# Optimization experiments

Hardware: AMD Instinct MI355X
Metric: run time of the kernel (lower is better)

The kernel has to match this reference:

```python
import jax, jax.numpy as jnp
import numpy as np

B = 8
IMG_H = 128
IMG_W = 128
C = 128
HEADS = 4
WS = 8
SHIFT = 4
HIDDEN = 512
EPS = 1e-5


def _rel_pos_index(ws):
    coords = np.stack(np.meshgrid(np.arange(ws), np.arange(ws), indexing='ij'))  # (2, ws, ws)
    cf = coords.reshape(2, -1)  # (2, N)
    rel = (cf[:, :, None] - cf[:, None, :]).transpose(1, 2, 0).copy()  # (N, N, 2)
    rel[:, :, 0] += ws - 1
    rel[:, :, 1] += ws - 1
    rel[:, :, 0] *= 2 * ws - 1
    return rel.sum(-1)  # (N, N) int


def _win_part_np(x, ws):
    b, h, w, c = x.shape
    x = x.reshape(b, h // ws, ws, w // ws, ws, c).transpose(0, 1, 3, 2, 4, 5)
    return x.reshape(-1, ws, ws, c)


def _attn_mask(H, W, ws, ss):
    img = np.zeros((1, H, W, 1), dtype=np.float32)
    slices = (slice(0, -ws), slice(-ws, -ss), slice(-ss, None))
    cnt = 0
    for hs in slices:
        for wsl in slices:
            img[:, hs, wsl, :] = cnt
            cnt += 1
    mw = _win_part_np(img, ws).reshape(-1, ws * ws)  # (nW, N)
    am = mw[:, None, :] - mw[:, :, None]  # (nW, N, N)
    return np.where(am != 0, np.float32(-100.0), np.float32(0.0))


def _layernorm(x, g, b):
    m = x.mean(-1, keepdims=True)
    v = ((x - m) ** 2).mean(-1, keepdims=True)
    return (x - m) / jnp.sqrt(v + EPS) * g + b


def setup_inputs() -> dict:
    key = jax.random.key(0)
    ks = jax.random.split(key, 8)
    s = 0.02
    return {
        'x': jax.random.normal(ks[0], (B, IMG_H * IMG_W, C), jnp.float32),
        'rpb_table': jax.random.normal(ks[1], ((2 * WS - 1) ** 2, HEADS), jnp.float32) * s,
        'norm1_g': jnp.ones((C,), jnp.float32),
        'norm1_b': jnp.zeros((C,), jnp.float32),
        'qkv_w': jax.random.normal(ks[2], (3 * C, C), jnp.float32) * s,
        'qkv_b': jnp.zeros((3 * C,), jnp.float32),
        'proj_w': jax.random.normal(ks[3], (C, C), jnp.float32) * s,
        'proj_b': jnp.zeros((C,), jnp.float32),
        'norm2_g': jnp.ones((C,), jnp.float32),
        'norm2_b': jnp.zeros((C,), jnp.float32),
        'fc1_w': jax.random.normal(ks[4], (HIDDEN, C), jnp.float32) * s,
        'fc1_b': jnp.zeros((HIDDEN,), jnp.float32),
        'fc2_w': jax.random.normal(ks[5], (C, HIDDEN), jnp.float32) * s,
        'fc2_b': jnp.zeros((C,), jnp.float32),
        'H': IMG_H,
        'W': IMG_W,
    }


def reference(x, rpb_table, norm1_g, norm1_b, qkv_w, qkv_b, proj_w, proj_b,
              norm2_g, norm2_b, fc1_w, fc1_b, fc2_w, fc2_b, H, W):
    Bx, L, Cx = x.shape
    nh, d, ws, ss = HEADS, C // HEADS, WS, SHIFT
    N = ws * ws
    shortcut = x
    h = _layernorm(x, norm1_g, norm1_b).reshape(Bx, H, W, Cx)
    # cyclic shift
    h = jnp.roll(h, (-ss, -ss), axis=(1, 2))
    # window partition -> (nW*B, N, C)
    h = h.reshape(Bx, H // ws, ws, W // ws, ws, Cx).transpose(0, 1, 3, 2, 4, 5).reshape(-1, N, Cx)
    # attention
    qkv = h @ qkv_w.T + qkv_b  # (nW*B, N, 3C)
    qkv = qkv.reshape(-1, N, 3, nh, d).transpose(2, 0, 3, 1, 4)  # (3, nW*B, nh, N, d)
    q, k, v = qkv[0] * (d ** -0.5), qkv[1], qkv[2]
    attn = jnp.einsum('whnd,whmd->whnm', q, k)  # (nW*B, nh, N, N)
    idx = _rel_pos_index(ws)
    bias = rpb_table[idx.reshape(-1)].reshape(N, N, nh).transpose(2, 0, 1)  # (nh, N, N)
    attn = attn + bias[None]
    mask = jnp.asarray(_attn_mask(H, W, ws, ss), x.dtype)  # (nW, N, N)
    nW = mask.shape[0]
    attn = attn.reshape(Bx, nW, nh, N, N) + mask[None, :, None]
    attn = jax.nn.softmax(attn.reshape(-1, nh, N, N), axis=-1)
    out = jnp.einsum('whnm,whmd->whnd', attn, v).transpose(0, 2, 1, 3).reshape(-1, N, Cx)
    out = out @ proj_w.T + proj_b
    # window reverse + reverse shift
    out = out.reshape(Bx, H // ws, W // ws, ws, ws, Cx).transpose(0, 1, 3, 2, 4, 5).reshape(Bx, H, W, Cx)
    out = jnp.roll(out, (ss, ss), axis=(1, 2)).reshape(Bx, H * W, Cx)
    x = shortcut + out
    # MLP with residual
    h2 = _layernorm(x, norm2_g, norm2_b)
    h2 = jax.nn.gelu(h2 @ fc1_w.T + fc1_b, approximate=False)
    h2 = h2 @ fc2_w.T + fc2_b
    return x + h2
```

## Files before the change

### kernel.cpp

```cpp
#include <hip/hip_runtime.h>
#include <math.h>

typedef unsigned short u16;
typedef unsigned int   u32;

#define SS_    4
#define NH     4
#define Dh     32
#define Cdim   128
#define Ntok   64
#define WTOT   2048
#define Mrows  131072
#define HIDDEN 512
#define PSTR   72
#define OSTR   136
#define HPAD   136

typedef __bf16 bf16x8 __attribute__((ext_vector_type(8)));
typedef u16    u16x8  __attribute__((ext_vector_type(8)));
typedef float  f32x4  __attribute__((ext_vector_type(4)));

__device__ __forceinline__ float bf2f(u16 u){
    union {u32 i; float f;} v; v.i = ((u32)u) << 16; return v.f;
}
__device__ __forceinline__ u16 f2bf(float f){
    union {float f; u32 i;} v; v.f = f;
    u32 x = v.i;
    return (u16)((x + 0x7fffu + ((x >> 16) & 1u)) >> 16);
}

__device__ __forceinline__ float fast_gelu(float v){
    float z = v * (1.5957691216057308f + 0.07135481627561976f * v * v);
    return v / (1.0f + __expf(-z));
}

__device__ __forceinline__ int map_row_to_token(int r){
    int w = r >> 6, n = r & 63;
    int b = w >> 8, win = w & 255;
    int wy = win >> 4, wx = win & 15;
    int iy = n >> 3, ix = n & 7;
    int ro = (wy*8 + iy + SS_) & 127;
    int co = (wx*8 + ix + SS_) & 127;
    return (b << 14) + (ro << 7) + co;
}

__device__ __forceinline__ int map_token_to_row(int t){
    int b = t >> 14, ro = (t >> 7) & 127, co = t & 127;
    int y  = (ro + 128 - SS_) & 127;
    int xq = (co + 128 - SS_) & 127;
    return (((b << 8) | ((y >> 3) << 4) | (xq >> 3)) << 6) + (y & 7)*8 + (xq & 7);
}

__global__ void __launch_bounds__(256) cvt_kernel(const float* __restrict__ src,
        u16* __restrict__ dst, int n)
{
    int i = blockIdx.x * 256 + threadIdx.x;
    if (i < n) dst[i] = f2bf(src[i]);
}

__global__ void __launch_bounds__(256) bm_kernel(const float* __restrict__ rpb,
        float* __restrict__ bmt)
{
    int e = blockIdx.x * 256 + threadIdx.x;
    int cls = e >> 14, h = (e >> 12) & 3, row = (e >> 6) & 63, col = e & 63;
    int iy = row >> 3, ix = row & 7, jy = col >> 3, jx = col & 7;
    int bidx = (iy - jy + 7)*15 + (ix - jx + 7);
    float bias = rpb[bidx*NH + h];
    int ybit = cls >> 1, xbit = cls & 1;
    int ri = (ybit ? (iy < 4 ? 1 : 2) : 0)*3 + (xbit ? (ix < 4 ? 1 : 2) : 0);
    int rj = (ybit ? (jy < 4 ? 1 : 2) : 0)*3 + (xbit ? (jx < 4 ? 1 : 2) : 0);
    bmt[e] = bias + ((ri != rj) ? -100.0f : 0.0f);
}

__global__ void __launch_bounds__(512, 4) ln1qkv_kernel(
        const float* __restrict__ x,
        const float* __restrict__ g, const float* __restrict__ bsh,
        const u16* __restrict__ Bw,
        const float* __restrict__ bias,
        u16* __restrict__ qb, u16* __restrict__ kb, u16* __restrict__ vb)
{
    __shared__ __align__(16) u16 Asm[128*HPAD];
    int t = threadIdx.x;
    size_t tilebase = (size_t)blockIdx.x * 128;

    #pragma unroll
    for (int it = 0; it < 4; it++){
        int idx = it*512 + t;
        int rr  = idx >> 4, c8 = idx & 15;
        int trow = (int)tilebase + rr;
        int src  = map_row_to_token(trow);
        f32x4 xa = *(const f32x4*)&x[(size_t)src*Cdim + c8*8];
        f32x4 xb = *(const f32x4*)&x[(size_t)src*Cdim + c8*8 + 4];
        float s = 0.0f, s2 = 0.0f;
        #pragma unroll
        for (int k = 0; k < 4; k++){
            s += xa[k] + xb[k];
            s2 += xa[k]*xa[k] + xb[k]*xb[k];
        }
        #pragma unroll
        for (int off = 1; off <= 8; off <<= 1){
            s  += __shfl_xor(s,  off, 64);
            s2 += __shfl_xor(s2, off, 64);
        }
        float mean = s * (1.0f/128.0f);
        float var  = s2 * (1.0f/128.0f) - mean*mean;
        float inv  = rsqrtf(var + 1e-5f);
        f32x4 ga = *(const f32x4*)&g[c8*8],  gb = *(const f32x4*)&g[c8*8 + 4];
        f32x4 ba = *(const f32x4*)&bsh[c8*8], bb = *(const f32x4*)&bsh[c8*8 + 4];
        u16x8 ov;
        #pragma unroll
        for (int k = 0; k < 4; k++){
            ov[k]   = f2bf((xa[k] - mean) * inv * ga[k] + ba[k]);
            ov[k+4] = f2bf((xb[k] - mean) * inv * gb[k] + bb[k]);
        }
        *(u16x8*)&Asm[rr*HPAD + c8*8] = ov;
    }
    __syncthreads();

    int wave = t >> 6, lane = t & 63;
    int wr = wave & 1, wc = wave >> 1;
    int m = lane & 15, quad = lane >> 4;

    #pragma unroll
    for (int pass = 0; pass < 2; pass++){
        int colbase = wc*96 + pass*48;
        f32x4 acc[4][3] = {};
        #pragma unroll
        for (int s = 0; s < 4; s++){
            bf16x8 aq[4], bk[3];
            #pragma unroll
            for (int i = 0; i < 4; i++)
                aq[i] = *(const bf16x8*)&Asm[(wr*64 + i*16 + m)*HPAD + s*32 + quad*8];
            #pragma unroll
            for (int j = 0; j < 3; j++)
                bk[j] = *(const bf16x8*)&Bw[(size_t)(colbase + j*16 + m)*Cdim
                                            + s*32 + quad*8];
            #pragma unroll
            for (int i = 0; i < 4; i++)
                #pragma unroll
                for (int j = 0; j < 3; j++)
                    acc[i][j] = __builtin_amdgcn_mfma_f32_16x16x32_bf16(
                                    aq[i], bk[j], acc[i][j], 0, 0, 0);
        }

        #pragma unroll
        for (int j = 0; j < 3; j++){
            int c = colbase + j*16 + m;
            float bia = bias[c];
            int which = c >> 7;
            int h = (c >> 5) & 3;
            int d = c & 31;
            #pragma unroll
            for (int i = 0; i < 4; i++){
                #pragma unroll
                for (int rg = 0; rg < 4; rg++){
                    int r = (int)tilebase + wr*64 + i*16 + quad*4 + rg;
                    float v = acc[i][j][rg] + bia;
                    int w = r >> 6, n = r & 63;
                    if (which == 0){
                        qb[((size_t)(w*NH + h)*Ntok + n)*Dh + d] =
                            f2bf(v * 0.17677669529663687f);
                    } else if (which == 1){
                        kb[((size_t)(w*NH + h)*Ntok + n)*Dh + d] = f2bf(v);
                    } else {
                        vb[((size_t)(w*NH + h)*Dh + d)*Ntok + n] = f2bf(v);
                    }
                }
            }
        }
    }
}

__global__ void __launch_bounds__(512, 4) mlp_kernel(
        const float* __restrict__ x,
        const u16* __restrict__ projout,
        const float* __restrict__ g, const float* __restrict__ bsh,
        const u16* __restrict__ W1,
        const float* __restrict__ b1,
        const u16* __restrict__ W2,
        const float* __restrict__ b2,
        float* __restrict__ outp)
{
    __shared__ __align__(16) u16 Asm[128*HPAD];
    __shared__ __align__(16) u16 Hsm[128*HPAD];
    int t = threadIdx.x;
    int wave = t >> 6, lane = t & 63;
    int wr = wave & 1, wc = wave >> 1;
    int m = lane & 15, quad = lane >> 4;
    size_t rowbase = (size_t)blockIdx.x * 128;

    #pragma unroll
    for (int it = 0; it < 4; it++){
        int idx  = it*512 + t;
        int r    = idx >> 4, c8 = idx & 15;
        int trow = (int)rowbase + r;
        int rr   = map_token_to_row(trow);
        f32x4 xa = *(const f32x4*)&x[(size_t)trow*Cdim + c8*8];
        f32x4 xb = *(const f32x4*)&x[(size_t)trow*Cdim + c8*8 + 4];
        u16x8 pv = *(const u16x8*)&projout[(size_t)rr*Cdim + c8*8];
        float val[8];
        float s = 0.0f, s2 = 0.0f;
        #pragma unroll
        for (int k = 0; k < 8; k++){
            float xv = (k < 4) ? xa[k] : xb[k-4];
            val[k] = xv + bf2f(pv[k]);
            s += val[k]; s2 += val[k]*val[k];
        }
        #pragma unroll
        for (int off = 1; off <= 8; off <<= 1){
            s  += __shfl_xor(s,  off, 64);
            s2 += __shfl_xor(s2, off, 64);
        }
        float mean = s * (1.0f/128.0f);
        float var  = s2 * (1.0f/128.0f) - mean*mean;
        float inv  = rsqrtf(var + 1e-5f);
        f32x4 ga = *(const f32x4*)&g[c8*8],  gb = *(const f32x4*)&g[c8*8 + 4];
        f32x4 ba = *(const f32x4*)&bsh[c8*8], bb = *(const f32x4*)&bsh[c8*8 + 4];
        u16x8 ov;
        #pragma unroll
        for (int k = 0; k < 8; k++){
            float gv = (k < 4) ? ga[k] : gb[k-4];
            float bv = (k < 4) ? ba[k] : bb[k-4];
            ov[k] = f2bf((val[k] - mean) * inv * gv + bv);
        }
        *(u16x8*)&Asm[r*HPAD + c8*8] = ov;
    }
    __syncthreads();

    f32x4 O[4][2] = {};

    for (int kk = 0; kk < 4; kk++){
        f32x4 Hacc[4][2] = {};
        #pragma unroll
        for (int s = 0; s < 4; s++){
            bf16x8 aq[4], bk[2];
            #pragma unroll
            for (int i = 0; i < 4; i++)
                aq[i] = *(const bf16x8*)&Asm[(wr*64 + i*16 + m)*HPAD + s*32 + quad*8];
            #pragma unroll
            for (int j = 0; j < 2; j++)
                bk[j] = *(const bf16x8*)&W1[(size_t)(kk*128 + wc*32 + j*16 + m)*Cdim
                                            + s*32 + quad*8];
            #pragma unroll
            for (int i = 0; i < 4; i++)
                #pragma unroll
                for (int j = 0; j < 2; j++)
                    Hacc[i][j] = __builtin_amdgcn_mfma_f32_16x16x32_bf16(
                                     aq[i], bk[j], Hacc[i][j], 0, 0, 0);
        }
        #pragma unroll
        for (int i = 0; i < 4; i++){
            #pragma unroll
            for (int j = 0; j < 2; j++){
                int hc = wc*32 + j*16 + m;
                float bia = b1[kk*128 + hc];
                #pragma unroll
                for (int rg = 0; rg < 4; rg++){
                    int r = wr*64 + i*16 + quad*4 + rg;
                    Hsm[r*HPAD + hc] = f2bf(fast_gelu(Hacc[i][j][rg] + bia));
                }
            }
        }
        __syncthreads();

        #pragma unroll
        for (int s = 0; s < 4; s++){
            bf16x8 pa[4], bk[2];
            #pragma unroll
            for (int i = 0; i < 4; i++)
                pa[i] = *(const bf16x8*)&Hsm[(wr*64 + i*16 + m)*HPAD + s*32 + quad*8];
            #pragma unroll
            for (int j = 0; j < 2; j++)
                bk[j] = *(const bf16x8*)&W2[(size_t)(wc*32 + j*16 + m)*HIDDEN
                                            + kk*128 + s*32 + quad*8];
            #pragma unroll
            for (int i = 0; i < 4; i++)
                #pragma unroll
                for (int j = 0; j < 2; j++)
                    O[i][j] = __builtin_amdgcn_mfma_f32_16x16x32_bf16(
                                  pa[i], bk[j], O[i][j], 0, 0, 0);
        }
        __syncthreads();
    }

    #pragma unroll
    for (int i = 0; i < 4; i++){
        #pragma unroll
        for (int rg = 0; rg < 4; rg++){
            int r  = (int)rowbase + wr*64 + i*16 + quad*4 + rg;
            int rr = map_token_to_row(r);
            #pragma unroll
            for (int j = 0; j < 2; j++){
                int c = wc*32 + j*16 + m;
                float v = x[(size_t)r*Cdim + c] + bf2f(projout[(size_t)rr*Cdim + c])
                          + O[i][j][rg] + b2[c];
                outp[(size_t)r*Cdim + c] = v;
            }
        }
    }
}

__global__ void __launch_bounds__(256) attnproj_kernel(
        const u16* __restrict__ qb, const u16* __restrict__ kb,
        const u16* __restrict__ vt, const float* __restrict__ bmt,
        const u16* __restrict__ pw, const float* __restrict__ pb,
        u16* __restrict__ projout)
{
    __shared__ __align__(16) u16 SH[NH*64*PSTR];
    int w = blockIdx.x;
    int win = w & 255;
    int wy = win >> 4, wx = win & 15;
    int cls = ((wy == 15) ? 2 : 0) | ((wx == 15) ? 1 : 0);
    int t = threadIdx.x;
    int h = t >> 6, lane = t & 63;
    int m = lane & 15, quad = lane >> 4;
    u16* Ph  = SH + h*64*PSTR;
    u16* Osm = SH;

    const u16* qg = qb + (size_t)(w*NH + h)*2048;
    const u16* kg = kb + (size_t)(w*NH + h)*2048;
    const u16* vg = vt + (size_t)(w*NH + h)*2048;
    const float* bm = bmt + (size_t)(cls*NH + h)*4096;

    bf16x8 aq[4], bk[4];
    #pragma unroll
    for (int i = 0; i < 4; i++)
        aq[i] = *(const bf16x8*)&qg[(i*16 + m)*32 + quad*8];
    #pragma unroll
    for (int j = 0; j < 4; j++)
        bk[j] = *(const bf16x8*)&kg[(j*16 + m)*32 + quad*8];
    f32x4 S[4][4] = {};
    #pragma unroll
    for (int i = 0; i < 4; i++)
        #pragma unroll
        for (int j = 0; j < 4; j++)
            S[i][j] = __builtin_amdgcn_mfma_f32_16x16x32_bf16(
                          aq[i], bk[j], S[i][j], 0, 0, 0);

    #pragma unroll
    for (int i = 0; i < 4; i++){
        #pragma unroll
        for (int rg = 0; rg < 4; rg++){
            int row = i*16 + quad*4 + rg;
            float s0 = S[i][0][rg] + bm[row*64 +  0 + m];
            float s1 = S[i][1][rg] + bm[row*64 + 16 + m];
            float s2 = S[i][2][rg] + bm[row*64 + 32 + m];
            float s3 = S[i][3][rg] + bm[row*64 + 48 + m];
            float mx = fmaxf(fmaxf(s0, s1), fmaxf(s2, s3));
            mx = fmaxf(mx, __shfl_xor(mx, 1, 64));
            mx = fmaxf(mx, __shfl_xor(mx, 2, 64));
            mx = fmaxf(mx, __shfl_xor(mx, 4, 64));
            mx = fmaxf(mx, __shfl_xor(mx, 8, 64));
            s0 = __expf(s0 - mx); s1 = __expf(s1 - mx);
            s2 = __expf(s2 - mx); s3 = __expf(s3 - mx);
            float sm = s0 + s1 + s2 + s3;
            sm += __shfl_xor(sm, 1, 64);
            sm += __shfl_xor(sm, 2, 64);
            sm += __shfl_xor(sm, 4, 64);
            sm += __shfl_xor(sm, 8, 64);
            float rinv = 1.0f / sm;
            u16* pr = &Ph[row*PSTR];
            pr[ 0 + m] = f2bf(s0 * rinv);
            pr[16 + m] = f2bf(s1 * rinv);
            pr[32 + m] = f2bf(s2 * rinv);
            pr[48 + m] = f2bf(s3 * rinv);
        }
    }

    f32x4 O[4][2] = {};
    #pragma unroll
    for (int s2 = 0; s2 < 2; s2++){
        bf16x8 pa[4], bv[2];
        #pragma unroll
        for (int i = 0; i < 4; i++)
            pa[i] = *(const bf16x8*)&Ph[(i*16 + m)*PSTR + s2*32 + quad*8];
        #pragma unroll
        for (int dt = 0; dt < 2; dt++)
            bv[dt] = *(const bf16x8*)&vg[(dt*16 + m)*64 + s2*32 + quad*8];
        #pragma unroll
        for (int i = 0; i < 4; i++)
            #pragma unroll
            for (int dt = 0; dt < 2; dt++)
                O[i][dt] = __builtin_amdgcn_mfma_f32_16x16x32_bf16(
                               pa[i], bv[dt], O[i][dt], 0, 0, 0);
    }

    __syncthreads();

    #pragma unroll
    for (int i = 0; i < 4; i++)
        #pragma unroll
        for (int dt = 0; dt < 2; dt++)
            #pragma unroll
            for (int rg = 0; rg < 4; rg++)
                Osm[(i*16 + quad*4 + rg)*OSTR + h*Dh + dt*16 + m] =
                    f2bf(O[i][dt][rg]);
    __syncthreads();

    f32x4 pacc[4][2] = {};
    #pragma unroll
    for (int s = 0; s < 4; s++){
        bf16x8 pa[4], pbk[2];
        #pragma unroll
        for (int i = 0; i < 4; i++)
            pa[i] = *(const bf16x8*)&Osm[(i*16 + m)*OSTR + s*32 + quad*8];
        #pragma unroll
        for (int j = 0; j < 2; j++)
            pbk[j] = *(const bf16x8*)&pw[(size_t)(h*Dh + j*16 + m)*Cdim
                                         + s*32 + quad*8];
        #pragma unroll
        for (int i = 0; i < 4; i++)
            #pragma unroll
            for (int j = 0; j < 2; j++)
                pacc[i][j] = __builtin_amdgcn_mfma_f32_16x16x32_bf16(
                                 pa[i], pbk[j], pacc[i][j], 0, 0, 0);
    }
    __syncthreads();

    #pragma unroll
    for (int i = 0; i < 4; i++)
        #pragma unroll
        for (int j = 0; j < 2; j++){
            int c = h*Dh + j*16 + m;
            float bia = pb[c];
            #pragma unroll
            for (int rg = 0; rg < 4; rg++)
                Osm[(i*16 + quad*4 + rg)*OSTR + c] = f2bf(pacc[i][j][rg] + bia);
        }
    __syncthreads();

    #pragma unroll
    for (int it = 0; it < 4; it++){
        int idx = it*256 + t;
        int r = idx >> 4, c16 = idx & 15;
        *(bf16x8*)&projout[((size_t)w*64 + r)*Cdim + c16*8] =
            *(const bf16x8*)&Osm[r*OSTR + c16*8];
    }
}

extern "C" void kernel_launch(void* const* d_in, const int* in_sizes, int n_in,
                              void* d_out, int out_size, void* d_ws, size_t ws_size,
                              hipStream_t stream) {
    const float* x     = (const float*)d_in[0];
    const float* rpb   = (const float*)d_in[1];
    const float* n1g   = (const float*)d_in[2];
    const float* n1b   = (const float*)d_in[3];
    const float* qkvw  = (const float*)d_in[4];
    const float* qkvb  = (const float*)d_in[5];
    const float* projw = (const float*)d_in[6];
    const float* projb = (const float*)d_in[7];
    const float* n2g   = (const float*)d_in[8];
    const float* n2b   = (const float*)d_in[9];
    const float* fc1w  = (const float*)d_in[10];
    const float* fc1b  = (const float*)d_in[11];
    const float* fc2w  = (const float*)d_in[12];
    const float* fc2b  = (const float*)d_in[13];
    float* out = (float*)d_out;

    if (ws_size < (size_t)230u * 1024u * 1024u) return;

    char* ws = (char*)d_ws;
    u16*  projout = (u16*)(ws);
    u16*  qbuf    = (u16*)(ws + ((size_t)32  << 20));
    u16*  kbuf    = (u16*)(ws + ((size_t)64  << 20));
    u16*  vbuf    = (u16*)(ws + ((size_t)96  << 20));
    u16*  wb      = (u16*)(ws + ((size_t)224 << 20));
    u16*  qkvw_b  = wb;
    u16*  projw_b = wb + 49152;
    u16*  fc1w_b  = wb + 65536;
    u16*  fc2w_b  = wb + 131072;
    float* bmt    = (float*)(ws + ((size_t)225 << 20));

    cvt_kernel<<<(49152+255)/256, 256, 0, stream>>>(qkvw, qkvw_b, 49152);
    cvt_kernel<<<(16384+255)/256, 256, 0, stream>>>(projw, projw_b, 16384);
    cvt_kernel<<<(65536+255)/256, 256, 0, stream>>>(fc1w, fc1w_b, 65536);
    cvt_kernel<<<(65536+255)/256, 256, 0, stream>>>(fc2w, fc2w_b, 65536);
    bm_kernel<<<256, 256, 0, stream>>>(rpb, bmt);

    ln1qkv_kernel<<<Mrows/128, 512, 0, stream>>>(
        x, n1g, n1b, qkvw_b, qkvb, qbuf, kbuf, vbuf);
    attnproj_kernel<<<WTOT, 256, 0, stream>>>(qbuf, kbuf, vbuf, bmt,
                                              projw_b, projb, projout);
    mlp_kernel<<<Mrows/128, 512, 0, stream>>>(
        x, projout, n2g, n2b, fc1w_b, fc1b, fc2w_b, fc2b, out);
}
```

Measured before the change: 375.0 us.

## Fuse LN1+QKV projection into the windowed attention kernel via shared memory

Merges the LayerNorm1+QKV GEMM kernel with the attention+projection kernel so each block handles one 64-token window. Q, K and V now stay in LDS instead of round-tripping through global memory, removing a kernel launch and about 100MB of global traffic. In exchange the QKV GEMM runs with 64-row tiles on 256 threads instead of 128-row tiles on 512 threads, so weight reuse per block drops. LDS use per block also rises to about 77KB, which limits occupancy.

After: 308.8 us. 17.6% less time.

```diff
diff --git a/kernel.cpp b/kernel.cpp
--- a/kernel.cpp
+++ b/kernel.cpp
@@ -12,9 +12,16 @@
 #define WTOT   2048
 #define Mrows  131072
 #define HIDDEN 512
-#define PSTR   72
+#define HPAD   136
+#define QKSTR  40
+#define VTSTR  72
+#define PSTR2  72
 #define OSTR   136
-#define HPAD   136
+
+#define SH_TOT  38400
+#define QOFF    8704
+#define KOFF    18944
+#define VOFF    29184
 
 typedef __bf16 bf16x8 __attribute__((ext_vector_type(8)));
 typedef u16    u16x8  __attribute__((ext_vector_type(8)));
@@ -72,23 +79,36 @@
     bmt[e] = bias + ((ri != rj) ? -100.0f : 0.0f);
 }
 
-__global__ void __launch_bounds__(512, 4) ln1qkv_kernel(
+__global__ void __launch_bounds__(256, 2) qkvattn_kernel(
         const float* __restrict__ x,
         const float* __restrict__ g, const float* __restrict__ bsh,
         const u16* __restrict__ Bw,
         const float* __restrict__ bias,
-        u16* __restrict__ qb, u16* __restrict__ kb, u16* __restrict__ vb)
+        const float* __restrict__ bmt,
+        const u16* __restrict__ pw, const float* __restrict__ pb,
+        u16* __restrict__ projout)
 {
-    __shared__ __align__(16) u16 Asm[128*HPAD];
+    __shared__ __align__(16) u16 SH[SH_TOT];
+    u16* Asm = SH;
+    u16* Qs  = SH + QOFF;
+    u16* Ks  = SH + KOFF;
+    u16* Vs  = SH + VOFF;
+    u16* Ps  = SH + QOFF;
+
     int t = threadIdx.x;
-    size_t tilebase = (size_t)blockIdx.x * 128;
+    int w = blockIdx.x;
+    int win = w & 255;
+    int wy = win >> 4, wx = win & 15;
+    int cls = ((wy == 15) ? 2 : 0) | ((wx == 15) ? 1 : 0);
+    int wv = t >> 6, lane = t & 63;
+    int m = lane & 15, quad = lane >> 4;
+    size_t tilebase = (size_t)w * 64;
 
     #pragma unroll
     for (int it = 0; it < 4; it++){
-        int idx = it*512 + t;
+        int idx = it*256 + t;
         int rr  = idx >> 4, c8 = idx & 15;
-        int trow = (int)tilebase + rr;
-        int src  = map_row_to_token(trow);
+        int src = map_row_to_token((int)tilebase + rr);
         f32x4 xa = *(const f32x4*)&x[(size_t)src*Cdim + c8*8];
         f32x4 xb = *(const f32x4*)&x[(size_t)src*Cdim + c8*8 + 4];
         float s = 0.0f, s2 = 0.0f;
@@ -117,20 +137,16 @@
     }
     __syncthreads();
 
-    int wave = t >> 6, lane = t & 63;
-    int wr = wave & 1, wc = wave >> 1;
-    int m = lane & 15, quad = lane >> 4;
-
     #pragma unroll
     for (int pass = 0; pass < 2; pass++){
-        int colbase = wc*96 + pass*48;
+        int colbase = pass*192 + wv*48;
         f32x4 acc[4][3] = {};
         #pragma unroll
         for (int s = 0; s < 4; s++){
             bf16x8 aq[4], bk[3];
             #pragma unroll
             for (int i = 0; i < 4; i++)
-                aq[i] = *(const bf16x8*)&Asm[(wr*64 + i*16 + m)*HPAD + s*32 + quad*8];
+                aq[i] = *(const bf16x8*)&Asm[(i*16 + m)*HPAD + s*32 + quad*8];
             #pragma unroll
             for (int j = 0; j < 3; j++)
                 bk[j] = *(const bf16x8*)&Bw[(size_t)(colbase + j*16 + m)*Cdim
@@ -142,7 +158,6 @@
                     acc[i][j] = __builtin_amdgcn_mfma_f32_16x16x32_bf16(
                                     aq[i], bk[j], acc[i][j], 0, 0, 0);
         }
-
         #pragma unroll
         for (int j = 0; j < 3; j++){
             int c = colbase + j*16 + m;
@@ -154,181 +169,30 @@
             for (int i = 0; i < 4; i++){
                 #pragma unroll
                 for (int rg = 0; rg < 4; rg++){
-                    int r = (int)tilebase + wr*64 + i*16 + quad*4 + rg;
+                    int n = i*16 + quad*4 + rg;
                     float v = acc[i][j][rg] + bia;
-                    int w = r >> 6, n = r & 63;
                     if (which == 0){
-                        qb[((size_t)(w*NH + h)*Ntok + n)*Dh + d] =
-                            f2bf(v * 0.17677669529663687f);
+                        Qs[(h*64 + n)*QKSTR + d] = f2bf(v * 0.17677669529663687f);
                     } else if (which == 1){
-                        kb[((size_t)(w*NH + h)*Ntok + n)*Dh + d] = f2bf(v);
+                        Ks[(h*64 + n)*QKSTR + d] = f2bf(v);
                     } else {
-                        vb[((size_t)(w*NH + h)*Dh + d)*Ntok + n] = f2bf(v);
+                        Vs[(h*32 + d)*VTSTR + n] = f2bf(v);
                     }
                 }
             }
         }
     }
-}
-
-__global__ void __launch_bounds__(512, 4) mlp_kernel(
-        const float* __restrict__ x,
-        const u16* __restrict__ projout,
-        const float* __restrict__ g, const float* __restrict__ bsh,
-        const u16* __restrict__ W1,
-        const float* __restrict__ b1,
-        const u16* __restrict__ W2,
-        const float* __restrict__ b2,
-        float* __restrict__ outp)
-{
-    __shared__ __align__(16) u16 Asm[128*HPAD];
-    __shared__ __align__(16) u16 Hsm[128*HPAD];
-    int t = threadIdx.x;
-    int wave = t >> 6, lane = t & 63;
-    int wr = wave & 1, wc = wave >> 1;
-    int m = lane & 15, quad = lane >> 4;
-    size_t rowbase = (size_t)blockIdx.x * 128;
-
-    #pragma unroll
-    for (int it = 0; it < 4; it++){
-        int idx  = it*512 + t;
-        int r    = idx >> 4, c8 = idx & 15;
-        int trow = (int)rowbase + r;
-        int rr   = map_token_to_row(trow);
-        f32x4 xa = *(const f32x4*)&x[(size_t)trow*Cdim + c8*8];
-        f32x4 xb = *(const f32x4*)&x[(size_t)trow*Cdim + c8*8 + 4];
-        u16x8 pv = *(const u16x8*)&projout[(size_t)rr*Cdim + c8*8];
-        float val[8];
-        float s = 0.0f, s2 = 0.0f;
-        #pragma unroll
-        for (int k = 0; k < 8; k++){
-            float xv = (k < 4) ? xa[k] : xb[k-4];
-            val[k] = xv + bf2f(pv[k]);
-            s += val[k]; s2 += val[k]*val[k];
-        }
-        #pragma unroll
-        for (int off = 1; off <= 8; off <<= 1){
-            s  += __shfl_xor(s,  off, 64);
-            s2 += __shfl_xor(s2, off, 64);
-        }
-        float mean = s * (1.0f/128.0f);
-        float var  = s2 * (1.0f/128.0f) - mean*mean;
-        float inv  = rsqrtf(var + 1e-5f);
-        f32x4 ga = *(const f32x4*)&g[c8*8],  gb = *(const f32x4*)&g[c8*8 + 4];
-        f32x4 ba = *(const f32x4*)&bsh[c8*8], bb = *(const f32x4*)&bsh[c8*8 + 4];
-        u16x8 ov;
-        #pragma unroll
-        for (int k = 0; k < 8; k++){
-            float gv = (k < 4) ? ga[k] : gb[k-4];
-            float bv = (k < 4) ? ba[k] : bb[k-4];
-            ov[k] = f2bf((val[k] - mean) * inv * gv + bv);
-        }
-        *(u16x8*)&Asm[r*HPAD + c8*8] = ov;
-    }
-    __syncthreads();
-
-    f32x4 O[4][2] = {};
-
-    for (int kk = 0; kk < 4; kk++){
-        f32x4 Hacc[4][2] = {};
-        #pragma unroll
-        for (int s = 0; s < 4; s++){
-            bf16x8 aq[4], bk[2];
-            #pragma unroll
-            for (int i = 0; i < 4; i++)
-                aq[i] = *(const bf16x8*)&Asm[(wr*64 + i*16 + m)*HPAD + s*32 + quad*8];
-            #pragma unroll
-            for (int j = 0; j < 2; j++)
-                bk[j] = *(const bf16x8*)&W1[(size_t)(kk*128 + wc*32 + j*16 + m)*Cdim
-                                            + s*32 + quad*8];
-            #pragma unroll
-            for (int i = 0; i < 4; i++)
-                #pragma unroll
-                for (int j = 0; j < 2; j++)
-                    Hacc[i][j] = __builtin_amdgcn_mfma_f32_16x16x32_bf16(
-                                     aq[i], bk[j], Hacc[i][j], 0, 0, 0);
-        }
-        #pragma unroll
-        for (int i = 0; i < 4; i++){
-            #pragma unroll
-            for (int j = 0; j < 2; j++){
-                int hc = wc*32 + j*16 + m;
-                float bia = b1[kk*128 + hc];
-                #pragma unroll
-                for (int rg = 0; rg < 4; rg++){
-                    int r = wr*64 + i*16 + quad*4 + rg;
-                    Hsm[r*HPAD + hc] = f2bf(fast_gelu(Hacc[i][j][rg] + bia));
-                }
-            }
-        }
-        __syncthreads();
-
-        #pragma unroll
-        for (int s = 0; s < 4; s++){
-            bf16x8 pa[4], bk[2];
-            #pragma unroll
-            for (int i = 0; i < 4; i++)
-                pa[i] = *(const bf16x8*)&Hsm[(wr*64 + i*16 + m)*HPAD + s*32 + quad*8];
-            #pragma unroll
-            for (int j = 0; j < 2; j++)
-                bk[j] = *(const bf16x8*)&W2[(size_t)(wc*32 + j*16 + m)*HIDDEN
-                                            + kk*128 + s*32 + quad*8];
-            #pragma unroll
-            for (int i = 0; i < 4; i++)
-                #pragma unroll
-                for (int j = 0; j < 2; j++)
-                    O[i][j] = __builtin_amdgcn_mfma_f32_16x16x32_bf16(
-                                  pa[i], bk[j], O[i][j], 0, 0, 0);
-        }
-        __syncthreads();
-    }
-
-    #pragma unroll
-    for (int i = 0; i < 4; i++){
-        #pragma unroll
-        for (int rg = 0; rg < 4; rg++){
-            int r  = (int)rowbase + wr*64 + i*16 + quad*4 + rg;
-            int rr = map_token_to_row(r);
-            #pragma unroll
-            for (int j = 0; j < 2; j++){
-                int c = wc*32 + j*16 + m;
-                float v = x[(size_t)r*Cdim + c] + bf2f(projout[(size_t)rr*Cdim + c])
-                          + O[i][j][rg] + b2[c];
-                outp[(size_t)r*Cdim + c] = v;
-            }
-        }
-    }
-}
-
-__global__ void __launch_bounds__(256) attnproj_kernel(
-        const u16* __restrict__ qb, const u16* __restrict__ kb,
-        const u16* __restrict__ vt, const float* __restrict__ bmt,
-        const u16* __restrict__ pw, const float* __restrict__ pb,
-        u16* __restrict__ projout)
-{
-    __shared__ __align__(16) u16 SH[NH*64*PSTR];
-    int w = blockIdx.x;
-    int win = w & 255;
-    int wy = win >> 4, wx = win & 15;
-    int cls = ((wy == 15) ? 2 : 0) | ((wx == 15) ? 1 : 0);
-    int t = threadIdx.x;
-    int h = t >> 6, lane = t & 63;
-    int m = lane & 15, quad = lane >> 4;
-    u16* Ph  = SH + h*64*PSTR;
-    u16* Osm = SH;
-
-    const u16* qg = qb + (size_t)(w*NH + h)*2048;
-    const u16* kg = kb + (size_t)(w*NH + h)*2048;
-    const u16* vg = vt + (size_t)(w*NH + h)*2048;
+    __syncthreads();
+
+    int h = wv;
     const float* bm = bmt + (size_t)(cls*NH + h)*4096;
-
     bf16x8 aq[4], bk[4];
     #pragma unroll
     for (int i = 0; i < 4; i++)
-        aq[i] = *(const bf16x8*)&qg[(i*16 + m)*32 + quad*8];
+        aq[i] = *(const bf16x8*)&Qs[(h*64 + i*16 + m)*QKSTR + quad*8];
     #pragma unroll
     for (int j = 0; j < 4; j++)
-        bk[j] = *(const bf16x8*)&kg[(j*16 + m)*32 + quad*8];
+        bk[j] = *(const bf16x8*)&Ks[(h*64 + j*16 + m)*QKSTR + quad*8];
     f32x4 S[4][4] = {};
     #pragma unroll
     for (int i = 0; i < 4; i++)
@@ -336,6 +200,7 @@
         for (int j = 0; j < 4; j++)
             S[i][j] = __builtin_amdgcn_mfma_f32_16x16x32_bf16(
                           aq[i], bk[j], S[i][j], 0, 0, 0);
+    __syncthreads();
 
     #pragma unroll
     for (int i = 0; i < 4; i++){
@@ -359,7 +224,7 @@
             sm += __shfl_xor(sm, 4, 64);
             sm += __shfl_xor(sm, 8, 64);
             float rinv = 1.0f / sm;
-            u16* pr = &Ph[row*PSTR];
+            u16* pr = &Ps[(h*64 + row)*PSTR2];
             pr[ 0 + m] = f2bf(s0 * rinv);
             pr[16 + m] = f2bf(s1 * rinv);
             pr[32 + m] = f2bf(s2 * rinv);
@@ -373,10 +238,10 @@
         bf16x8 pa[4], bv[2];
         #pragma unroll
         for (int i = 0; i < 4; i++)
-            pa[i] = *(const bf16x8*)&Ph[(i*16 + m)*PSTR + s2*32 + quad*8];
+            pa[i] = *(const bf16x8*)&Ps[(h*64 + i*16 + m)*PSTR2 + s2*32 + quad*8];
         #pragma unroll
         for (int dt = 0; dt < 2; dt++)
-            bv[dt] = *(const bf16x8*)&vg[(dt*16 + m)*64 + s2*32 + quad*8];
+            bv[dt] = *(const bf16x8*)&Vs[(h*32 + dt*16 + m)*VTSTR + s2*32 + quad*8];
         #pragma unroll
         for (int i = 0; i < 4; i++)
             #pragma unroll
@@ -385,8 +250,7 @@
                                pa[i], bv[dt], O[i][dt], 0, 0, 0);
     }
 
-    __syncthreads();
-
+    u16* Osm = Asm;
     #pragma unroll
     for (int i = 0; i < 4; i++)
         #pragma unroll
@@ -433,8 +297,137 @@
     for (int it = 0; it < 4; it++){
         int idx = it*256 + t;
         int r = idx >> 4, c16 = idx & 15;
-        *(bf16x8*)&projout[((size_t)w*64 + r)*Cdim + c16*8] =
+        *(bf16x8*)&projout[(tilebase + r)*Cdim + c16*8] =
             *(const bf16x8*)&Osm[r*OSTR + c16*8];
+    }
+}
+
+__global__ void __launch_bounds__(512, 4) mlp_kernel(
+        const float* __restrict__ x,
+        const u16* __restrict__ projout,
+        const float* __restrict__ g, const float* __restrict__ bsh,
+        const u16* __restrict__ W1,
+        const float* __restrict__ b1,
+        const u16* __restrict__ W2,
+        const float* __restrict__ b2,
+        float* __restrict__ outp)
+{
+    __shared__ __align__(16) u16 Asm[128*HPAD];
+    __shared__ __align__(16) u16 Hsm[128*HPAD];
+    int t = threadIdx.x;
+    int wave = t >> 6, lane = t & 63;
+    int wr = wave & 1, wc = wave >> 1;
+    int m = lane & 15, quad = lane >> 4;
+    size_t rowbase = (size_t)blockIdx.x * 128;
+
+    #pragma unroll
+    for (int it = 0; it < 4; it++){
+        int idx  = it*512 + t;
+        int r    = idx >> 4, c8 = idx & 15;
+        int trow = (int)rowbase + r;
+        int rr   = map_token_to_row(trow);
+        f32x4 xa = *(const f32x4*)&x[(size_t)trow*Cdim + c8*8];
+        f32x4 xb = *(const f32x4*)&x[(size_t)trow*Cdim + c8*8 + 4];
+        u16x8 pv = *(const u16x8*)&projout[(size_t)rr*Cdim + c8*8];
+        float val[8];
+        float s = 0.0f, s2 = 0.0f;
+        #pragma unroll
+        for (int k = 0; k < 8; k++){
+            float xv = (k < 4) ? xa[k] : xb[k-4];
+            val[k] = xv + bf2f(pv[k]);
+            s += val[k]; s2 += val[k]*val[k];
+        }
+        #pragma unroll
+        for (int off = 1; off <= 8; off <<= 1){
+            s  += __shfl_xor(s,  off, 64);
+            s2 += __shfl_xor(s2, off, 64);
+        }
+        float mean = s * (1.0f/128.0f);
+        float var  = s2 * (1.0f/128.0f) - mean*mean;
+        float inv  = rsqrtf(var + 1e-5f);
+        f32x4 ga = *(const f32x4*)&g[c8*8],  gb = *(const f32x4*)&g[c8*8 + 4];
+        f32x4 ba = *(const f32x4*)&bsh[c8*8], bb = *(const f32x4*)&bsh[c8*8 + 4];
+        u16x8 ov;
+        #pragma unroll
+        for (int k = 0; k < 8; k++){
+            float gv = (k < 4) ? ga[k] : gb[k-4];
+            float bv = (k < 4) ? ba[k] : bb[k-4];
+            ov[k] = f2bf((val[k] - mean) * inv * gv + bv);
+        }
+        *(u16x8*)&Asm[r*HPAD + c8*8] = ov;
+    }
+    __syncthreads();
+
+    f32x4 O[4][2] = {};
+
+    for (int kk = 0; kk < 4; kk++){
+        f32x4 Hacc[4][2] = {};
+        #pragma unroll
+        for (int s = 0; s < 4; s++){
+            bf16x8 aq[4], bk[2];
+            #pragma unroll
+            for (int i = 0; i < 4; i++)
+                aq[i] = *(const bf16x8*)&Asm[(wr*64 + i*16 + m)*HPAD + s*32 + quad*8];
+            #pragma unroll
+            for (int j = 0; j < 2; j++)
+                bk[j] = *(const bf16x8*)&W1[(size_t)(kk*128 + wc*32 + j*16 + m)*Cdim
+                                            + s*32 + quad*8];
+            #pragma unroll
+            for (int i = 0; i < 4; i++)
+                #pragma unroll
+                for (int j = 0; j < 2; j++)
+                    Hacc[i][j] = __builtin_amdgcn_mfma_f32_16x16x32_bf16(
+                                     aq[i], bk[j], Hacc[i][j], 0, 0, 0);
+        }
+        #pragma unroll
+        for (int i = 0; i < 4; i++){
+            #pragma unroll
+            for (int j = 0; j < 2; j++){
+                int hc = wc*32 + j*16 + m;
+                float bia = b1[kk*128 + hc];
+                #pragma unroll
+                for (int rg = 0; rg < 4; rg++){
+                    int r = wr*64 + i*16 + quad*4 + rg;
+                    Hsm[r*HPAD + hc] = f2bf(fast_gelu(Hacc[i][j][rg] + bia));
+                }
+            }
+        }
+        __syncthreads();
+
+        #pragma unroll
+        for (int s = 0; s < 4; s++){
+            bf16x8 pa[4], bk[2];
+            #pragma unroll
+            for (int i = 0; i < 4; i++)
+                pa[i] = *(const bf16x8*)&Hsm[(wr*64 + i*16 + m)*HPAD + s*32 + quad*8];
+            #pragma unroll
+            for (int j = 0; j < 2; j++)
+                bk[j] = *(const bf16x8*)&W2[(size_t)(wc*32 + j*16 + m)*HIDDEN
+                                            + kk*128 + s*32 + quad*8];
+            #pragma unroll
+            for (int i = 0; i < 4; i++)
+                #pragma unroll
+                for (int j = 0; j < 2; j++)
+                    O[i][j] = __builtin_amdgcn_mfma_f32_16x16x32_bf16(
+                                  pa[i], bk[j], O[i][j], 0, 0, 0);
+        }
+        __syncthreads();
+    }
+
+    #pragma unroll
+    for (int i = 0; i < 4; i++){
+        #pragma unroll
+        for (int rg = 0; rg < 4; rg++){
+            int r  = (int)rowbase + wr*64 + i*16 + quad*4 + rg;
+            int rr = map_token_to_row(r);
+            #pragma unroll
+            for (int j = 0; j < 2; j++){
+                int c = wc*32 + j*16 + m;
+                float v = x[(size_t)r*Cdim + c] + bf2f(projout[(size_t)rr*Cdim + c])
+                          + O[i][j][rg] + b2[c];
+                outp[(size_t)r*Cdim + c] = v;
+            }
+        }
     }
 }
 
@@ -461,9 +454,6 @@
 
     char* ws = (char*)d_ws;
     u16*  projout = (u16*)(ws);
-    u16*  qbuf    = (u16*)(ws + ((size_t)32  << 20));
-    u16*  kbuf    = (u16*)(ws + ((size_t)64  << 20));
-    u16*  vbuf    = (u16*)(ws + ((size_t)96  << 20));
     u16*  wb      = (u16*)(ws + ((size_t)224 << 20));
     u16*  qkvw_b  = wb;
     u16*  projw_b = wb + 49152;
@@ -477,10 +467,8 @@
     cvt_kernel<<<(65536+255)/256, 256, 0, stream>>>(fc2w, fc2w_b, 65536);
     bm_kernel<<<256, 256, 0, stream>>>(rpb, bmt);
 
-    ln1qkv_kernel<<<Mrows/128, 512, 0, stream>>>(
-        x, n1g, n1b, qkvw_b, qkvb, qbuf, kbuf, vbuf);
-    attnproj_kernel<<<WTOT, 256, 0, stream>>>(qbuf, kbuf, vbuf, bmt,
-                                              projw_b, projb, projout);
+    qkvattn_kernel<<<WTOT, 256, 0, stream>>>(
+        x, n1g, n1b, qkvw_b, qkvb, bmt, projw_b, projb, projout);
     mlp_kernel<<<Mrows/128, 512, 0, stream>>>(
         x, projout, n2g, n2b, fc1w_b, fc1b, fc2w_b, fc2b, out);
 }
```
